# Optimization experiments

Measured on AMD Instinct MI355X. Metric: run time of the kernel, lower is better.

Reference implementation:

```python
import jax, jax.numpy as jnp
import numpy as np

S, B, D_MODEL, H = 2048, 2, 1024, 16
DH = D_MODEL // H
SCALE = 1.0 / np.sqrt(DH)
NEG_INF = jnp.float32(-1e30)


def setup_inputs() -> dict:
    key = jax.random.key(0)
    ks = jax.random.split(key, 12)
    std = 1.0 / np.sqrt(D_MODEL)
    inp = {
        "query": jax.random.normal(ks[0], (S, B, D_MODEL), jnp.float32),
        "key": jax.random.normal(ks[1], (S, B, D_MODEL), jnp.float32),
        "value": jax.random.normal(ks[2], (S, B, D_MODEL), jnp.float32),
        # causal mask, shape (seq_q, seq_k, 1) per prepare_mask asserts
        "mask": jnp.tril(jnp.ones((S, S), dtype=bool))[:, :, None],
        # params stored (in, out) for x @ W
        "Wq": jax.random.normal(ks[3], (D_MODEL, H * DH), jnp.float32) * std,
        "bq": jnp.zeros((H * DH,), jnp.float32),
        "Wk": jax.random.normal(ks[4], (D_MODEL, H * DH), jnp.float32) * std,
        "bk": jnp.zeros((H * DH,), jnp.float32),
        "Wv": jax.random.normal(ks[5], (D_MODEL, H * DH), jnp.float32) * std,
        "bv": jnp.zeros((H * DH,), jnp.float32),
        "Wo": jax.random.normal(ks[6], (D_MODEL, D_MODEL), jnp.float32) * std,
        "bo": jnp.zeros((D_MODEL,), jnp.float32),
    }
    return inp


def reference(query, key, value, mask, Wq, bq, Wk, bk, Wv, bv, Wo, bo):
    seq_len, batch, _ = query.shape
    # project and split heads: (S, B, H, DH)
    q = (query @ Wq + bq).reshape(seq_len, batch, H, DH)
    k = (key @ Wk + bk).reshape(key.shape[0], batch, H, DH)
    v = (value @ Wv + bv).reshape(value.shape[0], batch, H, DH)
    # scores: (seq_q, batch, heads, seq_k)
    scores = jnp.einsum("ibhd,jbhd->ibhj", q, k) * SCALE
    # mask (seq_q, seq_k, batch_or_1) -> broadcast to (seq_q, batch, 1, seq_k)
    m = jnp.transpose(mask, (0, 2, 1))[:, :, None, :]
    scores = jnp.where(m, scores, NEG_INF)
    attn = jax.nn.softmax(scores, axis=-1)  # dropout_prob=0.0 (eval)
    x = jnp.einsum("ibhj,jbhd->ibhd", attn, v)
    x = x.reshape(seq_len, batch, H * DH)
    return x @ Wo + bo
```

## Files before the change

### kernel.cpp

```cpp
#include <hip/hip_runtime.h>
#include <hip/hip_bf16.h>
#include <cstdint>

#define S_LEN 2048
#define BATCH 2
#define DM    1024
#define NH    16
#define DH    64

typedef short s8v __attribute__((ext_vector_type(8)));
typedef float f4v __attribute__((ext_vector_type(4)));

__device__ __forceinline__ ushort f2bf(float x) {
  union { float f; uint32_t u; } v; v.f = x;
  uint32_t r = v.u + 0x7fffu + ((v.u >> 16) & 1u);
  return (ushort)(r >> 16);
}
__device__ __forceinline__ float bf2f(ushort u) {
  union { uint32_t u; float f; } v; v.u = (uint32_t)u << 16; return v.f;
}
__device__ __forceinline__ uint32_t fbits(float x) {
  union { float f; uint32_t u; } v; v.f = x; return v.u;
}
__device__ __forceinline__ uint32_t bfrnd(uint32_t u) {
  return u + 0x7fffu + ((u >> 16) & 1u);
}
__device__ __forceinline__ uint32_t packbf(uint32_t flo, uint32_t fhi) {
  return __builtin_amdgcn_perm(bfrnd(fhi), bfrnd(flo), 0x07060302u);
}
__device__ __forceinline__ uint32_t packbf_tr(float lo, float hi) {
  return __builtin_amdgcn_perm(fbits(hi), fbits(lo), 0x07060302u);
}

typedef __attribute__((address_space(1))) const void gas_void;
typedef __attribute__((address_space(3))) void las_void;
__device__ __forceinline__ void gld16(void* l, const void* g) {
  __builtin_amdgcn_global_load_lds((gas_void*)(uintptr_t)g,
                                   (las_void*)(uintptr_t)l, 16, 0, 0);
}

__global__ __launch_bounds__(256)
void prep(const float* W0, const float* W1, const float* W2, const float* W3,
          ushort* T0, ushort* T1, ushort* T2, ushort* T3,
          const float* X0, const float* X1, const float* X2,
          ushort* O0, ushort* O1, ushort* O2) {
  const int z = blockIdx.z;
  if (z < 4) {
    if (blockIdx.x >= 1024) return;
    const float* W = z == 0 ? W0 : z == 1 ? W1 : z == 2 ? W2 : W3;
    ushort*      T = z == 0 ? T0 : z == 1 ? T1 : z == 2 ? T2 : T3;
    __shared__ ushort tile[32][33];
    const int n0 = (blockIdx.x & 31) * 32, k0 = (blockIdx.x >> 5) * 32;
    const int tx = threadIdx.x & 31, ty = threadIdx.x >> 5;
    #pragma unroll
    for (int r = ty; r < 32; r += 8)
      tile[r][tx] = f2bf(W[(size_t)(k0 + r) * DM + n0 + tx]);
    __syncthreads();
    #pragma unroll
    for (int r = ty; r < 32; r += 8)
      T[(size_t)(n0 + r) * DM + k0 + tx] = tile[tx][r];
  } else {
    const float* X = z == 4 ? X0 : z == 5 ? X1 : X2;
    ushort*      O = z == 4 ? O0 : z == 5 ? O1 : O2;
    const size_t i = ((size_t)blockIdx.x * 256 + threadIdx.x) * 4;
    const float4 v = *(const float4*)(X + i);
    ushort4 h;
    h.x = f2bf(v.x); h.y = f2bf(v.y); h.z = f2bf(v.z); h.w = f2bf(v.w);
    *(ushort4*)(O + i) = h;
  }
}

__global__ __launch_bounds__(256)
void gemm_qkv(const ushort* __restrict__ Xq, const ushort* __restrict__ Xk,
              const ushort* __restrict__ Xv,
              const ushort* __restrict__ Wqt, const ushort* __restrict__ Wkt,
              const ushort* __restrict__ Wvt,
              const float* __restrict__ bq, const float* __restrict__ bk,
              const float* __restrict__ bv,
              ushort* __restrict__ Qh, ushort* __restrict__ Kh,
              ushort* __restrict__ Vt) {
  const int z = blockIdx.z;
  const ushort* A    = z == 0 ? Xq  : z == 1 ? Xk  : Xv;
  const ushort* Bt   = z == 0 ? Wqt : z == 1 ? Wkt : Wvt;
  const float*  bias = z == 0 ? bq  : z == 1 ? bk  : bv;

  __shared__ __align__(16) ushort lds[20480];

  const int tid = threadIdx.x, lane = tid & 63, w = tid >> 6;
  const int wr = w >> 1, wc = w & 1;
  const int lrow = lane & 15, quad = lane >> 4;
  const int m0 = blockIdx.x * 128, n0 = blockIdx.y * 128;

  const int sr4 = lane >> 2;
  const int scol = ((lane & 3) ^ (sr4 & 3)) * 8;

  const ushort* gA[2]; const ushort* gB[2];
  int oA[2], oB[2];
  #pragma unroll
  for (int t = 0; t < 2; t++) {
    const int c = 2 * w + t;
    gA[t] = A  + (size_t)(m0 + c * 16 + sr4) * DM + scol;
    oA[t] = c * 512;
    gB[t] = Bt + (size_t)(n0 + c * 16 + sr4) * DM + scol;
    oB[t] = 4096 + c * 512;
  }

  int pa[4], pb[4];
  #pragma unroll
  for (int i = 0; i < 4; i++) {
    pa[i] = (wr * 64 + i * 16 + lrow) * 32 + ((quad ^ (lrow & 3)) * 8);
    pb[i] = 4096 + (wc * 64 + i * 16 + lrow) * 32 + ((quad ^ (lrow & 3)) * 8);
  }

  f4v acc[4][4];
  #pragma unroll
  for (int i = 0; i < 4; i++)
    #pragma unroll
    for (int j = 0; j < 4; j++)
      acc[i][j] = f4v{0.f, 0.f, 0.f, 0.f};

  #pragma unroll
  for (int t = 0; t < 2; t++) {
    gld16(&lds[oA[t]], gA[t]);
    gld16(&lds[oB[t]], gB[t]);
  }

  for (int ks = 0; ks < 32; ks++) {
    __syncthreads();
    const int bo = (ks & 1) * 8192;
    if (ks < 31) {
      const int nb = ((ks + 1) & 1) * 8192;
      const int ko = (ks + 1) * 32;
      #pragma unroll
      for (int t = 0; t < 2; t++) {
        gld16(&lds[nb + oA[t]], gA[t] + ko);
        gld16(&lds[nb + oB[t]], gB[t] + ko);
      }
    }
    s8v af[4], bf[4];
    #pragma unroll
    for (int i = 0; i < 4; i++) af[i] = *(const s8v*)&lds[bo + pa[i]];
    #pragma unroll
    for (int j = 0; j < 4; j++) bf[j] = *(const s8v*)&lds[bo + pb[j]];
    #pragma unroll
    for (int i = 0; i < 4; i++)
      #pragma unroll
      for (int j = 0; j < 4; j++)
        acc[i][j] = __builtin_amdgcn_mfma_f32_16x16x32_bf16(af[i], bf[j], acc[i][j], 0, 0, 0);
  }

  if (z <= 1) {
    ushort* O = (z == 0) ? Qh : Kh;
    #pragma unroll
    for (int i = 0; i < 4; i++)
      #pragma unroll
      for (int j = 0; j < 4; j++) {
        const int n = n0 + wc * 64 + j * 16 + lrow;
        const float bval = bias[n];
        const int mb = m0 + wr * 64 + i * 16 + quad * 4;
        #pragma unroll
        for (int r = 0; r < 4; r++) {
          const int m = mb + r;
          const int s = m >> 1, b = m & 1;
          const int h = n >> 6, d = n & 63;
          O[((size_t)(b * NH + h) * S_LEN + s) * DH + d] = f2bf(acc[i][j][r] + bval);
        }
      }
  } else {
    __syncthreads();
    ushort* tw = lds + w * 5120;
    #pragma unroll
    for (int i = 0; i < 4; i++)
      #pragma unroll
      for (int j = 0; j < 4; j++) {
        const int n_l = j * 16 + lrow;
        const float bval = bias[n0 + wc * 64 + n_l];
        const int sbase = i * 8 + quad * 2;
        const uint32_t p0 = packbf(fbits(acc[i][j][0] + bval), fbits(acc[i][j][2] + bval));
        const uint32_t p1 = packbf(fbits(acc[i][j][1] + bval), fbits(acc[i][j][3] + bval));
        *(uint32_t*)&tw[n_l * 40 + sbase]        = p0;
        *(uint32_t*)&tw[2560 + n_l * 40 + sbase] = p1;
      }
    const int s0 = (m0 >> 1) + wr * 32;
    #pragma unroll
    for (int b = 0; b < 2; b++)
      #pragma unroll
      for (int p = 0; p < 4; p++) {
        const int d_l = p * 16 + (lane >> 2);
        const int c   = lane & 3;
        const s8v v = *(const s8v*)&tw[b * 2560 + d_l * 40 + c * 8];
        const int n = n0 + wc * 64 + d_l;
        const int h = n >> 6, d = n & 63;
        *(s8v*)&Vt[((size_t)(b * NH + h) * DH + d) * S_LEN + s0 + c * 8] = v;
      }
  }
}

__global__ __launch_bounds__(256)
void attn(const ushort* __restrict__ Qh, const ushort* __restrict__ Kh,
          const ushort* __restrict__ Vt, ushort* __restrict__ X,
          ushort* __restrict__ Opart, float* __restrict__ lpart) {
  __shared__ __align__(16) ushort Klds[2 * 64 * 64];
  __shared__ __align__(16) ushort Vlds[2 * 64 * 64];
  __shared__ __align__(16) ushort Plds[4][32 * 72];

  const int tid = threadIdx.x, lane = tid & 63, w = tid >> 6;
  const int lrow = lane & 15, quad = lane >> 4;
  const int bh = blockIdx.x;
  const int slot = blockIdx.y;
  int qt, part, nparts;
  if (slot < 18)      { qt = 15 - slot / 3;        part = slot % 3;        nparts = 3; }
  else if (slot < 30) { qt = 9  - (slot - 18) / 2; part = (slot - 18) % 2; nparts = 2; }
  else                { qt = 33 - slot;            part = 0;               nparts = 1; }
  const int nj  = 2 * qt + 2;
  const int jlo = part * nj / nparts;
  const int jhi = (part + 1) * nj / nparts;
  const int iw  = qt * 128 + w * 32;

  const int srow = lane >> 3;
  const int scol = ((lane & 7) ^ srow) * 8;
  const ushort* gK0 = Kh + ((size_t)bh * S_LEN + 2 * w * 8 + srow) * DH + scol;
  const ushort* gK1 = gK0 + 8 * DH;
  const ushort* gV0 = Vt + ((size_t)bh * DH + 2 * w * 8 + srow) * S_LEN + scol;
  const ushort* gV1 = gV0 + 8 * S_LEN;
  ushort* lK0 = &Klds[2 * w * 512]; ushort* lK1 = lK0 + 512;
  ushort* lV0 = &Vlds[2 * w * 512]; ushort* lV1 = lV0 + 512;

  s8v aq[2][2];
  #pragma unroll
  for (int is = 0; is < 2; is++)
    #pragma unroll
    for (int kk = 0; kk < 2; kk++)
      aq[is][kk] = *(const s8v*)(Qh + ((size_t)bh * S_LEN + iw + is * 16 + lrow) * DH +
                                 kk * 32 + quad * 8);

  const int f8 = lrow & 7;
  const ushort* pk[4][2]; const ushort* pv[4][2];
  #pragma unroll
  for (int s4 = 0; s4 < 4; s4++)
    #pragma unroll
    for (int kk = 0; kk < 2; kk++) {
      pk[s4][kk] = &Klds[(s4 * 16 + lrow) * 64 + (((kk * 4 + quad) ^ f8) * 8)];
      pv[s4][kk] = &Vlds[(s4 * 16 + lrow) * 64 + (((kk * 4 + quad) ^ f8) * 8)];
    }
  ushort* pwr = &Plds[w][lrow * 72];

  f4v o[2][4];
  float ls[2] = {0.f, 0.f};
  #pragma unroll
  for (int is = 0; is < 2; is++)
    #pragma unroll
    for (int d4 = 0; d4 < 4; d4++) o[is][d4] = f4v{0.f, 0.f, 0.f, 0.f};

  {
    const int b0 = (jlo & 1) * 4096;
    const size_t j0 = (size_t)jlo * 64;
    gld16(lK0 + b0, gK0 + j0 * DH);
    gld16(lK1 + b0, gK1 + j0 * DH);
    gld16(lV0 + b0, gV0 + j0);
    gld16(lV1 + b0, gV1 + j0);
  }

  for (int jt = jlo; jt < jhi; jt++) {
    const int j0 = jt * 64;
    __syncthreads();
    const int cur = (jt & 1) * 4096;
    if (jt + 1 < jhi) {
      const int nxt = ((jt + 1) & 1) * 4096;
      const size_t jn = (size_t)(jt + 1) * 64;
      gld16(lK0 + nxt, gK0 + jn * DH);
      gld16(lK1 + nxt, gK1 + jn * DH);
      gld16(lV0 + nxt, gV0 + jn);
      gld16(lV1 + nxt, gV1 + jn);
    }
    if (j0 > iw + 31) continue;

    f4v sc[2][4];
    #pragma unroll
    for (int is = 0; is < 2; is++)
      #pragma unroll
      for (int s4 = 0; s4 < 4; s4++) sc[is][s4] = f4v{0.f, 0.f, 0.f, 0.f};
    #pragma unroll
    for (int s4 = 0; s4 < 4; s4++) {
      const s8v k0f = *(const s8v*)(pk[s4][0] + cur);
      const s8v k1f = *(const s8v*)(pk[s4][1] + cur);
      sc[0][s4] = __builtin_amdgcn_mfma_f32_16x16x32_bf16(k0f, aq[0][0], sc[0][s4], 0, 0, 0);
      sc[1][s4] = __builtin_amdgcn_mfma_f32_16x16x32_bf16(k0f, aq[1][0], sc[1][s4], 0, 0, 0);
      sc[0][s4] = __builtin_amdgcn_mfma_f32_16x16x32_bf16(k1f, aq[0][1], sc[0][s4], 0, 0, 0);
      sc[1][s4] = __builtin_amdgcn_mfma_f32_16x16x32_bf16(k1f, aq[1][1], sc[1][s4], 0, 0, 0);
    }

    const bool needmask = (j0 + 63) > iw;
    #pragma unroll
    for (int is = 0; is < 2; is++) {
      const int ig = iw + is * 16 + lrow;
      #pragma unroll
      for (int s4 = 0; s4 < 4; s4++) {
        float e0 = __expf(sc[is][s4][0] * 0.125f);
        float e1 = __expf(sc[is][s4][1] * 0.125f);
        float e2 = __expf(sc[is][s4][2] * 0.125f);
        float e3 = __expf(sc[is][s4][3] * 0.125f);
        if (needmask) {
          const int jb = j0 + s4 * 16 + quad * 4;
          e0 = (jb + 0 > ig) ? 0.f : e0;
          e1 = (jb + 1 > ig) ? 0.f : e1;
          e2 = (jb + 2 > ig) ? 0.f : e2;
          e3 = (jb + 3 > ig) ? 0.f : e3;
        }
        ls[is] += (e0 + e1) + (e2 + e3);
        uint2 pk2;
        pk2.x = packbf_tr(e0, e1);
        pk2.y = packbf_tr(e2, e3);
        *(uint2*)&pwr[is * 16 * 72 + s4 * 16 + quad * 4] = pk2;
      }
    }

    s8v ap[2][2];
    #pragma unroll
    for (int is = 0; is < 2; is++)
      #pragma unroll
      for (int kt = 0; kt < 2; kt++)
        ap[is][kt] = *(const s8v*)&pwr[is * 16 * 72 + kt * 32 + quad * 8];
    #pragma unroll
    for (int d4 = 0; d4 < 4; d4++) {
      const s8v v0 = *(const s8v*)(pv[d4][0] + cur);
      const s8v v1 = *(const s8v*)(pv[d4][1] + cur);
      o[0][d4] = __builtin_amdgcn_mfma_f32_16x16x32_bf16(ap[0][0], v0, o[0][d4], 0, 0, 0);
      o[1][d4] = __builtin_amdgcn_mfma_f32_16x16x32_bf16(ap[1][0], v0, o[1][d4], 0, 0, 0);
      o[0][d4] = __builtin_amdgcn_mfma_f32_16x16x32_bf16(ap[0][1], v1, o[0][d4], 0, 0, 0);
      o[1][d4] = __builtin_amdgcn_mfma_f32_16x16x32_bf16(ap[1][1], v1, o[1][d4], 0, 0, 0);
    }
  }

  #pragma unroll
  for (int is = 0; is < 2; is++) {
    ls[is] += __shfl_xor(ls[is], 16, 64);
    ls[is] += __shfl_xor(ls[is], 32, 64);
  }

  if (nparts == 1) {
    const int bb = bh >> 4, h = bh & 15;
    #pragma unroll
    for (int is = 0; is < 2; is++)
      #pragma unroll
      for (int r = 0; r < 4; r++) {
        const float lv = __shfl(ls[is], quad * 16 + quad * 4 + r, 64);
        const float inv = 1.0f / lv;
        const int sg = iw + is * 16 + quad * 4 + r;
        #pragma unroll
        for (int d4 = 0; d4 < 4; d4++)
          X[((size_t)sg * BATCH + bb) * DM + h * DH + d4 * 16 + lrow] =
              f2bf(o[is][d4][r] * inv);
      }
  } else {
    ushort* Op = Opart + ((size_t)(bh * 30 + slot) * 128 + w * 32) * 64;
    #pragma unroll
    for (int is = 0; is < 2; is++)
      #pragma unroll
      for (int r = 0; r < 4; r++) {
        const int row_l = is * 16 + quad * 4 + r;
        #pragma unroll
        for (int d4 = 0; d4 < 4; d4++)
          Op[row_l * 64 + d4 * 16 + lrow] = f2bf(o[is][d4][r]);
      }
    if (quad == 0) {
      float* lp = lpart + (size_t)(bh * 30 + slot) * 128 + w * 32;
      lp[lrow]      = ls[0];
      lp[16 + lrow] = ls[1];
    }
  }
}

__global__ __launch_bounds__(256)
void combine(const ushort* __restrict__ Opart, const float* __restrict__ lpart,
             ushort* __restrict__ X) {
  const uint32_t gid = blockIdx.x * 256 + threadIdx.x;
  const int dv   = gid & 15;
  const int row  = (gid >> 4) & 127;
  const int rest = gid >> 11;
  const int qi   = rest % 12;
  const int bh   = rest / 12;
  const int qt   = 4 + qi;
  int s0, c;
  if (qt >= 10) { s0 = 3 * (15 - qt); c = 3; }
  else          { s0 = 18 + 2 * (9 - qt); c = 2; }

  float a0 = 0.f, a1 = 0.f, a2 = 0.f, a3 = 0.f, l = 0.f;
  #pragma unroll
  for (int p = 0; p < 3; p++) {
    if (p < c) {
      const size_t base = ((size_t)(bh * 30 + s0 + p) * 128 + row);
      const ushort4 v = *(const ushort4*)&Opart[base * 64 + dv * 4];
      a0 += bf2f(v.x); a1 += bf2f(v.y); a2 += bf2f(v.z); a3 += bf2f(v.w);
      l += lpart[base];
    }
  }
  const float inv = 1.0f / l;
  const int qpos = qt * 128 + row;
  const int b = bh >> 4, h = bh & 15;
  ushort4 hv;
  hv.x = f2bf(a0 * inv);
  hv.y = f2bf(a1 * inv);
  hv.z = f2bf(a2 * inv);
  hv.w = f2bf(a3 * inv);
  *(ushort4*)&X[(((size_t)qpos * BATCH + b) * NH + h) * DH + dv * 4] = hv;
}

__global__ __launch_bounds__(256)
void gemm_out(const ushort* __restrict__ A, const ushort* __restrict__ Bt,
              const float* __restrict__ bias, float* __restrict__ C) {
  __shared__ __align__(16) ushort lds[16384];

  const int tid = threadIdx.x, lane = tid & 63, w = tid >> 6;
  const int wr = w >> 1, wc = w & 1;
  const int lrow = lane & 15, quad = lane >> 4;
  const int m0 = blockIdx.x * 128, n0 = blockIdx.y * 128;

  const int sr4 = lane >> 2;
  const int scol = ((lane & 3) ^ (sr4 & 3)) * 8;

  const ushort* gA[2]; const ushort* gB[2];
  int oA[2], oB[2];
  #pragma unroll
  for (int t = 0; t < 2; t++) {
    const int c = 2 * w + t;
    gA[t] = A  + (size_t)(m0 + c * 16 + sr4) * DM + scol;
    oA[t] = c * 512;
    gB[t] = Bt + (size_t)(n0 + c * 16 + sr4) * DM + scol;
    oB[t] = 4096 + c * 512;
  }

  int pa[4], pb[4];
  #pragma unroll
  for (int i = 0; i < 4; i++) {
    pa[i] = (wr * 64 + i * 16 + lrow) * 32 + ((quad ^ (lrow & 3)) * 8);
    pb[i] = 4096 + (wc * 64 + i * 16 + lrow) * 32 + ((quad ^ (lrow & 3)) * 8);
  }

  f4v acc[4][4];
  #pragma unroll
  for (int i = 0; i < 4; i++)
    #pragma unroll
    for (int j = 0; j < 4; j++)
      acc[i][j] = f4v{0.f, 0.f, 0.f, 0.f};

  #pragma unroll
  for (int t = 0; t < 2; t++) {
    gld16(&lds[oA[t]], gA[t]);
    gld16(&lds[oB[t]], gB[t]);
  }

  for (int ks = 0; ks < 32; ks++) {
    __syncthreads();
    const int bo = (ks & 1) * 8192;
    if (ks < 31) {
      const int nb = ((ks + 1) & 1) * 8192;
      const int ko = (ks + 1) * 32;
      #pragma unroll
      for (int t = 0; t < 2; t++) {
        gld16(&lds[nb + oA[t]], gA[t] + ko);
        gld16(&lds[nb + oB[t]], gB[t] + ko);
      }
    }
    s8v af[4], bf[4];
    #pragma unroll
    for (int i = 0; i < 4; i++) af[i] = *(const s8v*)&lds[bo + pa[i]];
    #pragma unroll
    for (int j = 0; j < 4; j++) bf[j] = *(const s8v*)&lds[bo + pb[j]];
    #pragma unroll
    for (int i = 0; i < 4; i++)
      #pragma unroll
      for (int j = 0; j < 4; j++)
        acc[i][j] = __builtin_amdgcn_mfma_f32_16x16x32_bf16(af[i], bf[j], acc[i][j], 0, 0, 0);
  }

  #pragma unroll
  for (int i = 0; i < 4; i++)
    #pragma unroll
    for (int j = 0; j < 4; j++) {
      const int n = n0 + wc * 64 + j * 16 + lrow;
      const float bval = bias[n];
      const int mb = m0 + wr * 64 + i * 16 + quad * 4;
      #pragma unroll
      for (int r = 0; r < 4; r++)
        C[(size_t)(mb + r) * DM + n] = acc[i][j][r] + bval;
    }
}

extern "C" void kernel_launch(void* const* d_in, const int* in_sizes, int n_in,
                              void* d_out, int out_size, void* d_ws, size_t ws_size,
                              hipStream_t stream) {
  const float* query = (const float*)d_in[0];
  const float* key_  = (const float*)d_in[1];
  const float* value = (const float*)d_in[2];
  const float* Wq = (const float*)d_in[4];
  const float* bq = (const float*)d_in[5];
  const float* Wk = (const float*)d_in[6];
  const float* bk = (const float*)d_in[7];
  const float* Wv = (const float*)d_in[8];
  const float* bv = (const float*)d_in[9];
  const float* Wo = (const float*)d_in[10];
  const float* bo = (const float*)d_in[11];

  ushort* Wqt = (ushort*)d_ws;
  ushort* Wkt = Wqt + (size_t)1024 * 1024;
  ushort* Wvt = Wkt + (size_t)1024 * 1024;
  ushort* Wot = Wvt + (size_t)1024 * 1024;
  ushort* Xbq = Wot + (size_t)1024 * 1024;
  ushort* Xbk = Xbq + (size_t)4 * 1024 * 1024;
  ushort* Xbv = Xbk + (size_t)4 * 1024 * 1024;
  ushort* Qh  = Xbv + (size_t)4 * 1024 * 1024;
  ushort* Kh  = Qh  + (size_t)4 * 1024 * 1024;
  ushort* Vt  = Kh  + (size_t)4 * 1024 * 1024;
  ushort* Opart = Xbk;
  float*  lpart = (float*)Wqt;
  ushort* Xa  = Xbq;

  prep<<<dim3(4096, 1, 7), 256, 0, stream>>>(Wq, Wk, Wv, Wo, Wqt, Wkt, Wvt, Wot,
                                             query, key_, value, Xbq, Xbk, Xbv);
  gemm_qkv<<<dim3(32, 8, 3), 256, 0, stream>>>(Xbq, Xbk, Xbv,
                                               Wqt, Wkt, Wvt, bq, bk, bv,
                                               Qh, Kh, Vt);
  attn<<<dim3(32, 34), 256, 0, stream>>>(Qh, Kh, Vt, Xa, Opart, lpart);
  combine<<<3072, 256, 0, stream>>>(Opart, lpart, Xa);
  gemm_out<<<dim3(32, 8), 256, 0, stream>>>(Xa, Wot, bo, (float*)d_out);
}
```

Baseline: 235.6 us.

## Enlarge QKV GEMM tiles to 256x256 with four-stage LDS pipelining

The QKV projection GEMM moves from 128x128 tiles with 256 threads and double buffering to 256x256 tiles with 512 threads (8 waves). K-slices are streamed through a four-stage LDS ring with explicit vmcnt waits. Global loads are split and interleaved between two MFMA half-phases, with s_setprio raised around the MFMA bursts. This is meant to raise data reuse per block and hide load latency better. In exchange it uses 128KB of LDS per block and launches only 192 blocks, which may leave compute units idle and lower occupancy.

```diff
diff --git a/kernel.cpp b/kernel.cpp
--- a/kernel.cpp
+++ b/kernel.cpp
@@ -70,7 +70,7 @@
   }
 }
 
-__global__ __launch_bounds__(256)
+__global__ __launch_bounds__(512, 2)
 void gemm_qkv(const ushort* __restrict__ Xq, const ushort* __restrict__ Xk,
               const ushort* __restrict__ Xv,
               const ushort* __restrict__ Wqt, const ushort* __restrict__ Wkt,
@@ -84,115 +84,132 @@
   const ushort* Bt   = z == 0 ? Wqt : z == 1 ? Wkt : Wvt;
   const float*  bias = z == 0 ? bq  : z == 1 ? bk  : bv;
 
-  __shared__ __align__(16) ushort lds[20480];
+  __shared__ __align__(16) ushort lds[65536];
 
   const int tid = threadIdx.x, lane = tid & 63, w = tid >> 6;
-  const int wr = w >> 1, wc = w & 1;
+  const int wm = w >> 2, wn = w & 3;
   const int lrow = lane & 15, quad = lane >> 4;
-  const int m0 = blockIdx.x * 128, n0 = blockIdx.y * 128;
-
-  const int sr4 = lane >> 2;
-  const int scol = ((lane & 3) ^ (sr4 & 3)) * 8;
-
-  const ushort* gA[2]; const ushort* gB[2];
-  int oA[2], oB[2];
-  #pragma unroll
-  for (int t = 0; t < 2; t++) {
-    const int c = 2 * w + t;
-    gA[t] = A  + (size_t)(m0 + c * 16 + sr4) * DM + scol;
-    oA[t] = c * 512;
-    gB[t] = Bt + (size_t)(n0 + c * 16 + sr4) * DM + scol;
-    oB[t] = 4096 + c * 512;
-  }
-
-  int pa[4], pb[4];
-  #pragma unroll
-  for (int i = 0; i < 4; i++) {
-    pa[i] = (wr * 64 + i * 16 + lrow) * 32 + ((quad ^ (lrow & 3)) * 8);
-    pb[i] = 4096 + (wc * 64 + i * 16 + lrow) * 32 + ((quad ^ (lrow & 3)) * 8);
-  }
-
-  f4v acc[4][4];
-  #pragma unroll
-  for (int i = 0; i < 4; i++)
+  const int m0 = blockIdx.x * 256, n0 = blockIdx.y * 256;
+
+  const int tr = tid >> 2;
+  const int swz = ((tid & 3) ^ ((tid >> 3) & 3)) * 8;
+  const ushort* gA0 = A  + (size_t)(m0 + tr) * DM + swz;
+  const ushort* gA1 = A  + (size_t)(m0 + 128 + tr) * DM + swz;
+  const ushort* gB0 = Bt + (size_t)(n0 + tr) * DM + swz;
+  const ushort* gB1 = Bt + (size_t)(n0 + 128 + tr) * DM + swz;
+  const int dA0 = w * 512, dA1 = 4096 + w * 512;
+  const int dB0 = 8192 + w * 512, dB1 = 12288 + w * 512;
+
+  const int fr = (lrow >> 1) & 3;
+  int pa[8], pb[4];
+  #pragma unroll
+  for (int i = 0; i < 8; i++)
+    pa[i] = (wm * 128 + i * 16 + lrow) * 32 + ((quad ^ fr) * 8);
+  #pragma unroll
+  for (int j = 0; j < 4; j++)
+    pb[j] = 8192 + (wn * 64 + j * 16 + lrow) * 32 + ((quad ^ fr) * 8);
+
+  f4v acc[8][4];
+  #pragma unroll
+  for (int i = 0; i < 8; i++)
     #pragma unroll
     for (int j = 0; j < 4; j++)
       acc[i][j] = f4v{0.f, 0.f, 0.f, 0.f};
 
   #pragma unroll
-  for (int t = 0; t < 2; t++) {
-    gld16(&lds[oA[t]], gA[t]);
-    gld16(&lds[oB[t]], gB[t]);
-  }
-
-  for (int ks = 0; ks < 32; ks++) {
-    __syncthreads();
-    const int bo = (ks & 1) * 8192;
-    if (ks < 31) {
-      const int nb = ((ks + 1) & 1) * 8192;
-      const int ko = (ks + 1) * 32;
-      #pragma unroll
-      for (int t = 0; t < 2; t++) {
-        gld16(&lds[nb + oA[t]], gA[t] + ko);
-        gld16(&lds[nb + oB[t]], gB[t] + ko);
-      }
-    }
+  for (int t = 0; t < 3; t++) {
+    const int bb = t * 16384, ko = t * 32;
+    gld16(&lds[bb + dA0], gA0 + ko);
+    gld16(&lds[bb + dA1], gA1 + ko);
+    gld16(&lds[bb + dB0], gB0 + ko);
+    gld16(&lds[bb + dB1], gB1 + ko);
+  }
+  asm volatile("s_waitcnt vmcnt(8)" ::: "memory");
+  __builtin_amdgcn_s_barrier();
+
+  for (int t = 0; t < 32; t++) {
+    const int bb = (t & 3) * 16384;
+    const bool st = t < 29;
+    const int sbb = ((t + 3) & 3) * 16384;
+    const int ko = (t + 3) * 32;
     s8v af[4], bf[4];
     #pragma unroll
-    for (int i = 0; i < 4; i++) af[i] = *(const s8v*)&lds[bo + pa[i]];
-    #pragma unroll
-    for (int j = 0; j < 4; j++) bf[j] = *(const s8v*)&lds[bo + pb[j]];
+    for (int i = 0; i < 4; i++) af[i] = *(const s8v*)&lds[bb + pa[i]];
+    #pragma unroll
+    for (int j = 0; j < 4; j++) bf[j] = *(const s8v*)&lds[bb + pb[j]];
+    if (st) { gld16(&lds[sbb + dA0], gA0 + ko); gld16(&lds[sbb + dA1], gA1 + ko); }
+    __builtin_amdgcn_s_barrier();
+    __builtin_amdgcn_s_setprio(1);
     #pragma unroll
     for (int i = 0; i < 4; i++)
       #pragma unroll
       for (int j = 0; j < 4; j++)
         acc[i][j] = __builtin_amdgcn_mfma_f32_16x16x32_bf16(af[i], bf[j], acc[i][j], 0, 0, 0);
+    __builtin_amdgcn_s_setprio(0);
+    __builtin_amdgcn_s_barrier();
+    #pragma unroll
+    for (int i = 0; i < 4; i++) af[i] = *(const s8v*)&lds[bb + pa[4 + i]];
+    if (st) { gld16(&lds[sbb + dB0], gB0 + ko); gld16(&lds[sbb + dB1], gB1 + ko); }
+    __builtin_amdgcn_s_barrier();
+    __builtin_amdgcn_s_setprio(1);
+    #pragma unroll
+    for (int i = 0; i < 4; i++)
+      #pragma unroll
+      for (int j = 0; j < 4; j++)
+        acc[4 + i][j] = __builtin_amdgcn_mfma_f32_16x16x32_bf16(af[i], bf[j], acc[4 + i][j], 0, 0, 0);
+    __builtin_amdgcn_s_setprio(0);
+    if (t < 29)       asm volatile("s_waitcnt vmcnt(8)" ::: "memory");
+    else if (t == 29) asm volatile("s_waitcnt vmcnt(4)" ::: "memory");
+    else if (t == 30) asm volatile("s_waitcnt vmcnt(0)" ::: "memory");
+    __builtin_amdgcn_s_barrier();
   }
 
   if (z <= 1) {
     ushort* O = (z == 0) ? Qh : Kh;
     #pragma unroll
-    for (int i = 0; i < 4; i++)
+    for (int i = 0; i < 8; i++)
       #pragma unroll
       for (int j = 0; j < 4; j++) {
-        const int n = n0 + wc * 64 + j * 16 + lrow;
+        const int n = n0 + wn * 64 + j * 16 + lrow;
         const float bval = bias[n];
-        const int mb = m0 + wr * 64 + i * 16 + quad * 4;
+        const int h = n >> 6, d = n & 63;
+        const int mb = m0 + wm * 128 + i * 16 + quad * 4;
         #pragma unroll
         for (int r = 0; r < 4; r++) {
           const int m = mb + r;
-          const int s = m >> 1, b = m & 1;
-          const int h = n >> 6, d = n & 63;
-          O[((size_t)(b * NH + h) * S_LEN + s) * DH + d] = f2bf(acc[i][j][r] + bval);
+          O[((size_t)((m & 1) * NH + h) * S_LEN + (m >> 1)) * DH + d] = f2bf(acc[i][j][r] + bval);
         }
       }
   } else {
-    __syncthreads();
     ushort* tw = lds + w * 5120;
-    #pragma unroll
-    for (int i = 0; i < 4; i++)
-      #pragma unroll
-      for (int j = 0; j < 4; j++) {
-        const int n_l = j * 16 + lrow;
-        const float bval = bias[n0 + wc * 64 + n_l];
-        const int sbase = i * 8 + quad * 2;
-        const uint32_t p0 = packbf(fbits(acc[i][j][0] + bval), fbits(acc[i][j][2] + bval));
-        const uint32_t p1 = packbf(fbits(acc[i][j][1] + bval), fbits(acc[i][j][3] + bval));
-        *(uint32_t*)&tw[n_l * 40 + sbase]        = p0;
-        *(uint32_t*)&tw[2560 + n_l * 40 + sbase] = p1;
-      }
-    const int s0 = (m0 >> 1) + wr * 32;
-    #pragma unroll
-    for (int b = 0; b < 2; b++)
-      #pragma unroll
-      for (int p = 0; p < 4; p++) {
-        const int d_l = p * 16 + (lane >> 2);
-        const int c   = lane & 3;
-        const s8v v = *(const s8v*)&tw[b * 2560 + d_l * 40 + c * 8];
-        const int n = n0 + wc * 64 + d_l;
-        const int h = n >> 6, d = n & 63;
-        *(s8v*)&Vt[((size_t)(b * NH + h) * DH + d) * S_LEN + s0 + c * 8] = v;
-      }
+    const int h = (n0 + wn * 64) >> 6;
+    const int s0b = (m0 + wm * 128) >> 1;
+    #pragma unroll
+    for (int mh = 0; mh < 2; mh++) {
+      #pragma unroll
+      for (int i = 0; i < 4; i++)
+        #pragma unroll
+        for (int j = 0; j < 4; j++) {
+          const int d_l = j * 16 + lrow;
+          const float bval = bias[n0 + wn * 64 + d_l];
+          const f4v a = acc[mh * 4 + i][j];
+          const int sbase = i * 8 + quad * 2;
+          const uint32_t p0 = packbf(fbits(a[0] + bval), fbits(a[2] + bval));
+          const uint32_t p1 = packbf(fbits(a[1] + bval), fbits(a[3] + bval));
+          *(uint32_t*)&tw[d_l * 40 + sbase]        = p0;
+          *(uint32_t*)&tw[2560 + d_l * 40 + sbase] = p1;
+        }
+      const int s0 = s0b + mh * 32;
+      #pragma unroll
+      for (int b = 0; b < 2; b++)
+        #pragma unroll
+        for (int p = 0; p < 4; p++) {
+          const int d_l = p * 16 + (lane >> 2);
+          const int c   = lane & 3;
+          const s8v v = *(const s8v*)&tw[b * 2560 + d_l * 40 + c * 8];
+          *(s8v*)&Vt[((size_t)(b * NH + h) * DH + d_l) * S_LEN + s0 + c * 8] = v;
+        }
+    }
   }
 }
 
@@ -518,7 +535,7 @@
 
   prep<<<dim3(4096, 1, 7), 256, 0, stream>>>(Wq, Wk, Wv, Wo, Wqt, Wkt, Wvt, Wot,
                                              query, key_, value, Xbq, Xbk, Xbv);
-  gemm_qkv<<<dim3(32, 8, 3), 256, 0, stream>>>(Xbq, Xbk, Xbv,
+  gemm_qkv<<<dim3(16, 4, 3), 512, 0, stream>>>(Xbq, Xbk, Xbv,
                                                Wqt, Wkt, Wvt, bq, bk, bv,
                                                Qh, Kh, Vt);
   attn<<<dim3(32, 34), 256, 0, stream>>>(Qh, Kh, Vt, Xa, Opart, lpart);
```

Result: faster. 230.9 us (-2.0%).
